# Kernel tuning notes

Hardware: AMD Instinct MI355X
Metric: run time of the kernel (lower is better)

## Reference

```python
import jax, jax.numpy as jnp
import numpy as np

N = 51200      # total nodes
E = 1638400    # total edges (avg degree 32)
G = 512        # graphs in batch
IN = 16        # input node features
H = 4          # heads
C = 32         # channels per head
HC = H * C     # 128, concat output width
SLOPE = 0.2    # LeakyReLU negative slope
BN_EPS = 1e-5


def _glorot(k, shape, fan):
    return jax.random.normal(k, shape, jnp.float32) / np.sqrt(fan).astype(np.float32)


def setup_inputs() -> dict:
    key = jax.random.key(0)
    ks = jax.random.split(key, 32)
    inp = {}
    inp['x'] = jax.random.normal(ks[0], (N, IN), jnp.float32)
    inp['edge_index'] = jax.random.randint(ks[1], (2, E), 0, N)
    inp['batch'] = jnp.sort(jax.random.randint(ks[2], (N,), 0, G))
    # GATv2 layer 1 (IN -> H*C)
    inp['l1_Wl'] = _glorot(ks[3], (IN, HC), IN)
    inp['l1_bl'] = jnp.zeros((HC,), jnp.float32)
    inp['l1_Wr'] = _glorot(ks[4], (IN, HC), IN)
    inp['l1_br'] = jnp.zeros((HC,), jnp.float32)
    inp['l1_att'] = _glorot(ks[5], (H, C), C)
    inp['l1_bias'] = jnp.zeros((HC,), jnp.float32)
    # GATv2 layer 2 (HC -> H*C)
    inp['l2_Wl'] = _glorot(ks[6], (HC, HC), HC)
    inp['l2_bl'] = jnp.zeros((HC,), jnp.float32)
    inp['l2_Wr'] = _glorot(ks[7], (HC, HC), HC)
    inp['l2_br'] = jnp.zeros((HC,), jnp.float32)
    inp['l2_att'] = _glorot(ks[8], (H, C), C)
    inp['l2_bias'] = jnp.zeros((HC,), jnp.float32)
    # MLP head (HC -> HC -> HC -> 2) with BatchNorm (eval mode, running stats 0/1)
    inp['fc1_W'] = _glorot(ks[9], (HC, HC), HC)
    inp['fc1_b'] = jnp.zeros((HC,), jnp.float32)
    inp['bn1_g'] = jnp.ones((HC,), jnp.float32)
    inp['bn1_b'] = jnp.zeros((HC,), jnp.float32)
    inp['fc2_W'] = _glorot(ks[10], (HC, HC), HC)
    inp['fc2_b'] = jnp.zeros((HC,), jnp.float32)
    inp['bn2_g'] = jnp.ones((HC,), jnp.float32)
    inp['bn2_b'] = jnp.zeros((HC,), jnp.float32)
    inp['fc3_W'] = _glorot(ks[11], (HC, 2), HC)
    inp['fc3_b'] = jnp.zeros((2,), jnp.float32)
    return inp


def gatv2_conv(x, src, dst, Wl, bl, Wr, br, att, bias):
    # PyG GATv2Conv (share_weights=False, concat=True), eval mode (no dropout).
    xl = (x @ Wl + bl).reshape(-1, H, C)  # source transform  [N,H,C]
    xr = (x @ Wr + br).reshape(-1, H, C)  # target transform  [N,H,C]
    e = jax.nn.leaky_relu(xl[src] + xr[dst], SLOPE)   # [E,H,C]
    score = jnp.einsum('ehc,hc->eh', e, att)          # [E,H]
    # segment softmax over edges sharing the same target node
    m = jax.ops.segment_max(score, dst, num_segments=N)
    ex = jnp.exp(score - m[dst])
    denom = jax.ops.segment_sum(ex, dst, num_segments=N)
    alpha = ex / (denom[dst] + 1e-16)                 # [E,H]
    out = jax.ops.segment_sum(xl[src] * alpha[:, :, None], dst, num_segments=N)
    return out.reshape(-1, HC) + bias


def reference(x, edge_index, batch,
              l1_Wl, l1_bl, l1_Wr, l1_br, l1_att, l1_bias,
              l2_Wl, l2_bl, l2_Wr, l2_br, l2_att, l2_bias,
              fc1_W, fc1_b, bn1_g, bn1_b,
              fc2_W, fc2_b, bn2_g, bn2_b,
              fc3_W, fc3_b):
    src, dst = edge_index[0], edge_index[1]
    h = jax.nn.relu(gatv2_conv(x, src, dst, l1_Wl, l1_bl, l1_Wr, l1_br, l1_att, l1_bias))
    h = jax.nn.relu(gatv2_conv(h, src, dst, l2_Wl, l2_bl, l2_Wr, l2_br, l2_att, l2_bias))
    # global mean pool over graphs
    s = jax.ops.segment_sum(h, batch, num_segments=G)
    cnt = jax.ops.segment_sum(jnp.ones((N,), h.dtype), batch, num_segments=G)
    g = s / jnp.maximum(cnt, 1.0)[:, None]            # [G,HC]
    # MLP head; BatchNorm1d in eval mode with running_mean=0, running_var=1
    def bn(z, gamma, beta):
        return z * (gamma / np.sqrt(1.0 + BN_EPS).astype(np.float32)) + beta
    g = jax.nn.relu(bn(g @ fc1_W + fc1_b, bn1_g, bn1_b))
    g = jax.nn.relu(bn(g @ fc2_W + fc2_b, bn2_g, bn2_b))
    return g @ fc3_W + fc3_b                          # [G,2]
```

## Files before the change

### kernel.cpp

```cpp
#include <hip/hip_runtime.h>
#include <math.h>

#define NN 51200
#define EE 1638400
#define GG 512
#define INF 16
#define HCC 128
#define NB 400
#define TILE 4096
#define CSRCAP 4608
#define NBLK8 (NN / 8)

typedef float vf2 __attribute__((ext_vector_type(2)));
typedef short v8s __attribute__((ext_vector_type(8)));
typedef float v4f __attribute__((ext_vector_type(4)));
typedef _Float16 vh8 __attribute__((ext_vector_type(8)));
typedef float vf8 __attribute__((ext_vector_type(8)));
#define FMA2 __builtin_elementwise_fma
#define MIN2 __builtin_elementwise_min
#define MAX2 __builtin_elementwise_max


__device__ __forceinline__ int wave_incl_scan(int v, int lane) {
#pragma unroll
    for (int d = 1; d < 64; d <<= 1) {
        int y = __shfl_up(v, d);
        if (lane >= d) v += y;
    }
    return v;
}

__device__ __forceinline__ unsigned short bf16_rtne(float f) {
    unsigned u = __builtin_bit_cast(unsigned, f);
    unsigned r = u + 0x7FFFu + ((u >> 16) & 1u);
    return (unsigned short)(r >> 16);
}

__device__ __forceinline__ unsigned short f16_rtne(float f) {
    return __builtin_bit_cast(unsigned short, (_Float16)f);
}

__device__ __forceinline__ float dpp_xor1(float x) {
    int y = __builtin_amdgcn_mov_dpp(__builtin_bit_cast(int, x), 0xB1, 0xF, 0xF, true);
    return __builtin_bit_cast(float, y);
}
__device__ __forceinline__ float dpp_xor2(float x) {
    int y = __builtin_amdgcn_mov_dpp(__builtin_bit_cast(int, x), 0x4E, 0xF, 0xF, true);
    return __builtin_bit_cast(float, y);
}

__global__ __launch_bounds__(512) void k_hist(const int* __restrict__ ei,
                                              int* __restrict__ bcnt) {
    __shared__ int h[NB];
    int t = threadIdx.x;
    if (t < NB) h[t] = 0;
    __syncthreads();
    int e0 = blockIdx.x * TILE;
#pragma unroll
    for (int s = 0; s < 8; s++) {
        int d = ei[EE + e0 + s * 512 + t];
        atomicAdd(&h[d >> 7], 1);
    }
    __syncthreads();
    if (t < NB && h[t]) atomicAdd(&bcnt[t], h[t]);
}

__global__ __launch_bounds__(512) void k_scan2(const int* __restrict__ bcnt,
                                               int* __restrict__ bbase,
                                               int* __restrict__ gcur,
                                               int* __restrict__ rowptr) {
    __shared__ int sc[512];
    int t = threadIdx.x;
    int v = (t < NB) ? bcnt[t] : 0;
    sc[t] = v;
    __syncthreads();
    for (int off = 1; off < 512; off <<= 1) {
        int u = (t >= off) ? sc[t - off] : 0;
        __syncthreads();
        sc[t] += u;
        __syncthreads();
    }
    if (t < NB) { int ex = sc[t] - v; bbase[t] = ex; gcur[t] = ex; }
    if (t == 0) { bbase[NB] = EE; rowptr[NN] = EE; }
}

__global__ __launch_bounds__(512) void k_binlin1(const int* __restrict__ ei,
                                                 int* __restrict__ gcur,
                                                 unsigned* __restrict__ binned,
                                                 const float* __restrict__ x,
                                                 const float* __restrict__ Wl,
                                                 const float* __restrict__ bl,
                                                 const float* __restrict__ Wr,
                                                 const float* __restrict__ br,
                                                 unsigned short* __restrict__ xl,
                                                 float* __restrict__ xr,
                                                 const float* __restrict__ W2l,
                                                 const float* __restrict__ W2r,
                                                 unsigned short* __restrict__ Bhi,
                                                 unsigned short* __restrict__ Blo) {
    __shared__ int h[512];
    __shared__ int lexcl[NB], lcur[NB], baseg[NB];
    __shared__ unsigned stage[TILE];
    __shared__ int wsum[8];
    __shared__ float sx[4][INF];
    int t = threadIdx.x;
    if (blockIdx.x < NB) {
        int lane = t & 63, w = t >> 6;
        h[t] = 0;
        __syncthreads();
        int e0 = blockIdx.x * TILE;
        int sv[8], dv[8];
#pragma unroll
        for (int s = 0; s < 8; s++) {
            int e = e0 + s * 512 + t;
            sv[s] = ei[e];
            dv[s] = ei[EE + e];
            atomicAdd(&h[dv[s] >> 7], 1);
        }
        __syncthreads();
        int myh = h[t];
        int incl = wave_incl_scan(myh, lane);
        if (lane == 63) wsum[w] = incl;
        __syncthreads();
        int woff = 0;
        for (int i = 0; i < w; i++) woff += wsum[i];
        incl += woff;
        if (t < NB) {
            int ex = incl - myh;
            lexcl[t] = ex;
            lcur[t] = ex;
            baseg[t] = atomicAdd(&gcur[t], myh);
        }
        __syncthreads();
#pragma unroll
        for (int s = 0; s < 8; s++) {
            int b = dv[s] >> 7;
            int r = atomicAdd(&lcur[b], 1);
            stage[r] = (unsigned)sv[s] | ((unsigned)dv[s] << 16);
        }
        __syncthreads();
#pragma unroll
        for (int s = 0; s < 8; s++) {
            int idx = s * 512 + t;
            unsigned p = stage[idx];
            int b = (int)(p >> 23);
            binned[baseg[b] + idx - lexcl[b]] = p;
        }
    } else if (blockIdx.x < NB + NN / 4) {
        int bid = blockIdx.x - NB;
        int j = t & 127;
        int ty = t >> 7;
        int row = bid * 4 + ty;
        if (t < 64) {
            sx[t >> 4][t & 15] = x[(size_t)(bid * 4 + (t >> 4)) * INF + (t & 15)];
        }
        __syncthreads();
        float al = bl[j], ar = br[j];
#pragma unroll
        for (int k = 0; k < INF; k++) {
            float xv = sx[ty][k];
            al = fmaf(xv, Wl[k * HCC + j], al);
            ar = fmaf(xv, Wr[k * HCC + j], ar);
        }
        int head = j >> 5, ch = j & 31;
        xl[((size_t)(head >> 1) * NN + row) * 64 + (head & 1) * 32 + ch] = f16_rtne(al);
        xr[((size_t)head * NN + row) * 32 + ch] = ar;
    } else {
        int gt = (blockIdx.x - NB - NN / 4) * 512 + t;
        int ks = gt >> 10;
        int rem = gt & 1023;
        int nt = rem >> 6;
        int lane = rem & 63;
        int n = nt * 16 + (lane & 15);
        int kbase = ks * 32 + (lane >> 4) * 8;
        const float* src = (n < 128) ? (W2l + n) : (W2r + n - 128);
        unsigned short hi8[8], lo8[8];
#pragma unroll
        for (int j = 0; j < 8; j++) {
            float v = src[(size_t)(kbase + j) * HCC];
            unsigned short hb = bf16_rtne(v);
            float hf = __builtin_bit_cast(float, (unsigned)hb << 16);
            hi8[j] = hb;
            lo8[j] = bf16_rtne(v - hf);
        }
        size_t idx = (size_t)gt * 8;
#pragma unroll
        for (int j = 0; j < 8; j++) { Bhi[idx + j] = hi8[j]; Blo[idx + j] = lo8[j]; }
    }
}

__global__ __launch_bounds__(512) void k_csr(const unsigned* __restrict__ binned,
                                             const int* __restrict__ bbase,
                                             int* __restrict__ rowptr,
                                             int* __restrict__ col) {
    int b = blockIdx.x;
    int base = bbase[b];
    int cnt = bbase[b + 1] - base;
    __shared__ int nh[1024], ncur[1024];
    __shared__ unsigned sbin[CSRCAP];
    __shared__ int wsum[8];
    int t = threadIdx.x;
    int lane = t & 63, w = t >> 6;
    nh[t] = 0;
    nh[t + 512] = 0;
    __syncthreads();
    for (int e = t; e < cnt; e += 512) {
        unsigned p = binned[base + e];
        if (e < CSRCAP) sbin[e] = p;
        unsigned src = p & 0xFFFFu;
        int key = (int)(((p >> 16) & 127u) << 3) | (int)(src >> 13);
        atomicAdd(&nh[key], 1);
    }
    __syncthreads();
    int c0 = nh[2 * t], c1 = nh[2 * t + 1];
    int tot = c0 + c1;
    int incl = wave_incl_scan(tot, lane);
    if (lane == 63) wsum[w] = incl;
    __syncthreads();
    int woff = 0;
    for (int i = 0; i < w; i++) woff += wsum[i];
    int tex = incl + woff - tot;
    ncur[2 * t] = base + tex;
    ncur[2 * t + 1] = base + tex + c0;
    if ((t & 3) == 0) rowptr[(b << 7) + (t >> 2)] = base + tex;
    __syncthreads();
    for (int e = t; e < cnt; e += 512) {
        unsigned p = (e < CSRCAP) ? sbin[e] : binned[base + e];
        unsigned src = p & 0xFFFFu;
        int key = (int)(((p >> 16) & 127u) << 3) | (int)(src >> 13);
        int r = atomicAdd(&ncur[key], 1);
        col[r] = (int)src;
    }
}

__global__ __launch_bounds__(256) void k_lin2(const float* __restrict__ hin,
                                              const unsigned short* __restrict__ Bhi,
                                              const unsigned short* __restrict__ Blo,
                                              const float* __restrict__ bl,
                                              const float* __restrict__ br,
                                              unsigned short* __restrict__ outl,
                                              float* __restrict__ outr) {
    const int tid = threadIdx.x;
    const int wv = tid >> 6;
    const int lane = tid & 63;
    const int m = lane & 15;
    const int quad = lane >> 4;
    const int r0 = blockIdx.x * 64 + wv * 16;
    const float* arow = hin + (size_t)(r0 + m) * HCC + quad * 8;
    const v8s* bh = (const v8s*)Bhi;
    const v8s* bo = (const v8s*)Blo;

    v4f acc[16];
#pragma unroll
    for (int nt = 0; nt < 16; nt++) acc[nt] = (v4f){0.f, 0.f, 0.f, 0.f};

#pragma unroll
    for (int ks = 0; ks < 4; ks++) {
        const float4 av0 = *(const float4*)(arow + ks * 32);
        const float4 av1 = *(const float4*)(arow + ks * 32 + 4);
        const float af[8] = {av0.x, av0.y, av0.z, av0.w, av1.x, av1.y, av1.z, av1.w};
        v8s ahi, alo;
#pragma unroll
        for (int e = 0; e < 8; e++) {
            unsigned short hb = bf16_rtne(af[e]);
            float hf = __builtin_bit_cast(float, (unsigned)hb << 16);
            ahi[e] = (short)hb;
            alo[e] = (short)bf16_rtne(af[e] - hf);
        }
        const int base = ks * 16 * 64 + lane;
#pragma unroll
        for (int nt = 0; nt < 16; nt++) {
            v8s bhv = bh[base + nt * 64];
            v8s blv = bo[base + nt * 64];
            acc[nt] = __builtin_amdgcn_mfma_f32_16x16x32_bf16(ahi, bhv, acc[nt], 0, 0, 0);
            acc[nt] = __builtin_amdgcn_mfma_f32_16x16x32_bf16(ahi, blv, acc[nt], 0, 0, 0);
            acc[nt] = __builtin_amdgcn_mfma_f32_16x16x32_bf16(alo, bhv, acc[nt], 0, 0, 0);
        }
    }
#pragma unroll
    for (int nt = 0; nt < 16; nt++) {
        int n = nt * 16 + m;
        int c = n & 127;
        float bv = (n < 128) ? bl[c] : br[c];
        if (n < 128) {
            int head = c >> 5, ch = c & 31;
            unsigned short* op = outl + (size_t)(head >> 1) * NN * 64 + (head & 1) * 32 + ch;
#pragma unroll
            for (int r = 0; r < 4; r++) {
                int row = r0 + quad * 4 + r;
                op[(size_t)row * 64] = f16_rtne(acc[nt][r] + bv);
            }
        } else {
            float* op = outr + (size_t)(c >> 5) * NN * 32 + (c & 31);
#pragma unroll
            for (int r = 0; r < 4; r++) {
                int row = r0 + quad * 4 + r;
                op[(size_t)row * 32] = acc[nt][r] + bv;
            }
        }
    }
}

__global__ __launch_bounds__(512) void k_attn(const int* __restrict__ rowptr,
                                              const int* __restrict__ col,
                                              const unsigned short* __restrict__ xl,
                                              const float* __restrict__ xr,
                                              const float* __restrict__ att,
                                              const float* __restrict__ bias,
                                              float* __restrict__ hout) {
    const int wave = threadIdx.x >> 6;
    const int lane = threadIdx.x & 63;
    const int sub = lane >> 3;
    const int hl = (lane >> 2) & 1;
    const int hq = lane & 3;
    const int pair = blockIdx.x / NBLK8;
    const int n = (blockIdx.x - pair * NBLK8) * 8 + wave;
    const int head = 2 * pair + hl;

    const char* xlq = (const char*)(xl + (size_t)pair * NN * 64)
                      + (unsigned)(hl * 64 + hq * 16);
    const float* xrp = xr + ((size_t)head * NN + n) * 32 + hq * 8;
    const float4 xrv0 = *(const float4*)(xrp);
    const float4 xrv1 = *(const float4*)(xrp + 4);
    const float4 at0 = *(const float4*)(att + head * 32 + hq * 8);
    const float4 at1 = *(const float4*)(att + head * 32 + hq * 8 + 4);
    const float LOG2E = 1.44269504088896340736f;
    const vf2 xr01 = {xrv0.x, xrv0.y}, xr23 = {xrv0.z, xrv0.w};
    const vf2 xr45 = {xrv1.x, xrv1.y}, xr67 = {xrv1.z, xrv1.w};
    const vf2 at01 = {at0.x * LOG2E, at0.y * LOG2E}, at23 = {at0.z * LOG2E, at0.w * LOG2E};
    const vf2 at45 = {at1.x * LOG2E, at1.y * LOG2E}, at67 = {at1.z * LOG2E, at1.w * LOG2E};
    const vf2 Z2 = {0.f, 0.f}, C2 = {0.2f, 0.2f};

    const int base = rowptr[n];
    const int deg = rowptr[n + 1] - base;

    float l = 0.f;
    vf2 a01 = Z2, a23 = Z2, a45 = Z2, a67 = Z2;

    for (int i0 = 0; i0 < deg; i0 += 64) {
        int mye = 0;
        if (i0 + lane < deg) mye = col[base + i0 + lane];
        const int cnt = min(64, deg - i0);
        const int events = (cnt + 15) >> 4;
        vh8 ca, cb, na{}, nb{};
        {
            const int s0 = __shfl(mye, sub);
            const int s1 = __shfl(mye, 8 + sub);
            ca = *(const vh8*)(xlq + (((unsigned)s0) << 7));
            cb = *(const vh8*)(xlq + (((unsigned)s1) << 7));
        }
        for (int g = 0; g < events; ++g) {
            if (g + 1 < events) {
                const int s0 = __shfl(mye, 16 * (g + 1) + sub);
                const int s1 = __shfl(mye, 16 * (g + 1) + 8 + sub);
                na = *(const vh8*)(xlq + (((unsigned)s0) << 7));
                nb = *(const vh8*)(xlq + (((unsigned)s1) << 7));
            }
#pragma unroll
            for (int k = 0; k < 2; ++k) {
                const vf8 fv = __builtin_convertvector(k ? cb : ca, vf8);
                const vf2 v01 = {fv[0], fv[1]}, v23 = {fv[2], fv[3]};
                const vf2 v45 = {fv[4], fv[5]}, v67 = {fv[6], fv[7]};
                vf2 e, kk, p2;
                e = v01 + xr01; kk = FMA2(C2, MIN2(e, Z2), MAX2(e, Z2)); p2 = kk * at01;
                e = v23 + xr23; kk = FMA2(C2, MIN2(e, Z2), MAX2(e, Z2)); p2 = FMA2(kk, at23, p2);
                e = v45 + xr45; kk = FMA2(C2, MIN2(e, Z2), MAX2(e, Z2)); p2 = FMA2(kk, at45, p2);
                e = v67 + xr67; kk = FMA2(C2, MIN2(e, Z2), MAX2(e, Z2)); p2 = FMA2(kk, at67, p2);
                float pp = p2.x + p2.y;
                pp += dpp_xor1(pp);
                pp += dpp_xor2(pp);
                if ((16 * g + 8 * k + sub) >= cnt) pp = -INFINITY;
                const float w = __builtin_amdgcn_exp2f(pp);
                l += w;
                const vf2 W = {w, w};
                a01 = FMA2(W, v01, a01);
                a23 = FMA2(W, v23, a23);
                a45 = FMA2(W, v45, a45);
                a67 = FMA2(W, v67, a67);
            }
            ca = na;
            cb = nb;
        }
    }
    l += __shfl_xor(l, 8);
    l += __shfl_xor(l, 16);
    l += __shfl_xor(l, 32);
    float af[8] = {a01.x, a01.y, a23.x, a23.y, a45.x, a45.y, a67.x, a67.y};
#pragma unroll
    for (int i = 0; i < 8; i++) {
        af[i] += __shfl_xor(af[i], 8);
        af[i] += __shfl_xor(af[i], 16);
        af[i] += __shfl_xor(af[i], 32);
    }
    const float inv = 1.f / (l + 1e-16f);
    if (sub == 0) {
        const float4 b0 = *(const float4*)(bias + head * 32 + hq * 8);
        const float4 b1 = *(const float4*)(bias + head * 32 + hq * 8 + 4);
        float4 o0, o1;
        o0.x = fmaxf(fmaf(af[0], inv, b0.x), 0.f);
        o0.y = fmaxf(fmaf(af[1], inv, b0.y), 0.f);
        o0.z = fmaxf(fmaf(af[2], inv, b0.z), 0.f);
        o0.w = fmaxf(fmaf(af[3], inv, b0.w), 0.f);
        o1.x = fmaxf(fmaf(af[4], inv, b1.x), 0.f);
        o1.y = fmaxf(fmaf(af[5], inv, b1.y), 0.f);
        o1.z = fmaxf(fmaf(af[6], inv, b1.z), 0.f);
        o1.w = fmaxf(fmaf(af[7], inv, b1.w), 0.f);
        float* hp = hout + (size_t)n * HCC + head * 32 + hq * 8;
        *(float4*)(hp) = o0;
        *(float4*)(hp + 4) = o1;
    }
}

__global__ __launch_bounds__(128) void k_head(const float* __restrict__ h,
                                              const int* __restrict__ batch,
                                              const float* __restrict__ fc1W, const float* __restrict__ fc1b,
                                              const float* __restrict__ bn1g, const float* __restrict__ bn1b,
                                              const float* __restrict__ fc2W, const float* __restrict__ fc2b,
                                              const float* __restrict__ bn2g, const float* __restrict__ bn2b,
                                              const float* __restrict__ fc3W, const float* __restrict__ fc3b,
                                              float* __restrict__ out) {
    int g = blockIdx.x;
    int j = threadIdx.x;
    __shared__ float buf[HCC], buf2[HCC];
    int lo = 0, hi = NN;
    while (lo < hi) { int mid = (lo + hi) >> 1; if (batch[mid] < g) lo = mid + 1; else hi = mid; }
    int s = lo;
    lo = 0; hi = NN;
    while (lo < hi) { int mid = (lo + hi) >> 1; if (batch[mid] < g + 1) lo = mid + 1; else hi = mid; }
    int e = lo;
    float s0 = 0.f, s1 = 0.f, s2 = 0.f, s3 = 0.f;
    int n = s;
    for (; n + 3 < e; n += 4) {
        s0 += h[(size_t)n * HCC + j];
        s1 += h[(size_t)(n + 1) * HCC + j];
        s2 += h[(size_t)(n + 2) * HCC + j];
        s3 += h[(size_t)(n + 3) * HCC + j];
    }
    for (; n < e; n++) s0 += h[(size_t)n * HCC + j];
    float sum = (s0 + s1) + (s2 + s3);
    float cnt = (float)(e - s);
    buf[j] = sum / fmaxf(cnt, 1.0f);
    __syncthreads();
    const float SQ = 1.00000499998749994f;
    float a = fc1b[j];
    for (int k = 0; k < HCC; k++) a = fmaf(buf[k], fc1W[k * HCC + j], a);
    a = fmaf(a, bn1g[j] / SQ, bn1b[j]);
    a = fmaxf(a, 0.f);
    buf2[j] = a;
    __syncthreads();
    a = fc2b[j];
    for (int k = 0; k < HCC; k++) a = fmaf(buf2[k], fc2W[k * HCC + j], a);
    a = fmaf(a, bn2g[j] / SQ, bn2b[j]);
    a = fmaxf(a, 0.f);
    buf[j] = a;
    __syncthreads();
    if (j < 2) {
        float o = fc3b[j];
        for (int k = 0; k < HCC; k++) o = fmaf(buf[k], fc3W[k * 2 + j], o);
        out[g * 2 + j] = o;
    }
}

extern "C" void kernel_launch(void* const* d_in, const int* in_sizes, int n_in,
                              void* d_out, int out_size, void* d_ws, size_t ws_size,
                              hipStream_t stream) {
    const float* x      = (const float*)d_in[0];
    const int*   ei     = (const int*)d_in[1];
    const int*   batch  = (const int*)d_in[2];
    const float* l1_Wl  = (const float*)d_in[3];
    const float* l1_bl  = (const float*)d_in[4];
    const float* l1_Wr  = (const float*)d_in[5];
    const float* l1_br  = (const float*)d_in[6];
    const float* l1_att = (const float*)d_in[7];
    const float* l1_bias= (const float*)d_in[8];
    const float* l2_Wl  = (const float*)d_in[9];
    const float* l2_bl  = (const float*)d_in[10];
    const float* l2_Wr  = (const float*)d_in[11];
    const float* l2_br  = (const float*)d_in[12];
    const float* l2_att = (const float*)d_in[13];
    const float* l2_bias= (const float*)d_in[14];
    const float* fc1_W  = (const float*)d_in[15];
    const float* fc1_b  = (const float*)d_in[16];
    const float* bn1_g  = (const float*)d_in[17];
    const float* bn1_b  = (const float*)d_in[18];
    const float* fc2_W  = (const float*)d_in[19];
    const float* fc2_b  = (const float*)d_in[20];
    const float* bn2_g  = (const float*)d_in[21];
    const float* bn2_b  = (const float*)d_in[22];
    const float* fc3_W  = (const float*)d_in[23];
    const float* fc3_b  = (const float*)d_in[24];
    float* out = (float*)d_out;

    unsigned short* xlh = (unsigned short*)d_ws;
    float* xr = (float*)(xlh + (size_t)NN * HCC);
    float* h  = xr + (size_t)NN * HCC;
    int* rowptr = (int*)(h + (size_t)NN * HCC);
    int* col    = rowptr + (NN + 1);
    int* bcnt   = col + EE;
    int* bbase  = bcnt + NB;
    int* gcur   = bbase + (NB + 1);
    uintptr_t bp = ((uintptr_t)(gcur + NB) + 15) & ~(uintptr_t)15;
    unsigned short* Bhi = (unsigned short*)bp;
    unsigned short* Blo = Bhi + 32768;
    unsigned* binned = (unsigned*)h;

    hipMemsetAsync(bcnt, 0, NB * sizeof(int), stream);
    k_hist<<<EE / TILE, 512, 0, stream>>>(ei, bcnt);
    k_scan2<<<1, 512, 0, stream>>>(bcnt, bbase, gcur, rowptr);
    k_binlin1<<<NB + NN / 4 + 8, 512, 0, stream>>>(ei, gcur, binned,
                                                   x, l1_Wl, l1_bl, l1_Wr, l1_br, xlh, xr,
                                                   l2_Wl, l2_Wr, Bhi, Blo);
    k_csr<<<NB, 512, 0, stream>>>(binned, bbase, rowptr, col);

    k_attn<<<2 * NBLK8, 512, 0, stream>>>(rowptr, col, xlh, xr, l1_att, l1_bias, h);

    k_lin2<<<NN / 64, 256, 0, stream>>>(h, Bhi, Blo, l2_bl, l2_br, xlh, xr);
    k_attn<<<2 * NBLK8, 512, 0, stream>>>(rowptr, col, xlh, xr, l2_att, l2_bias, h);

    k_head<<<GG, 128, 0, stream>>>(h, batch, fc1_W, fc1_b, bn1_g, bn1_b,
                                   fc2_W, fc2_b, bn2_g, bn2_b, fc3_W, fc3_b, out);
}
```

Before: 426.0 us.

## Precompute graph bounds, batch lin1 rows per block, use DPP for xor-8 reductions

The single-block scan kernel now also derives per-graph node boundaries from the sorted batch array. The head kernel reads those boundaries instead of running two serial binary searches per graph. The layer-1 linear blocks each process 16 rows instead of 4, which cuts block count and reuses the weight loads. The attention kernel's xor-8 lane reductions use a DPP row rotate instead of a shuffle. Together these trim small overheads, but they add a serial loop over all nodes to the one-block scan kernel.

Result: slower. 450.9 us (+5.9%).

```diff
diff --git a/kernel.cpp b/kernel.cpp
--- a/kernel.cpp
+++ b/kernel.cpp
@@ -48,6 +48,10 @@
     int y = __builtin_amdgcn_mov_dpp(__builtin_bit_cast(int, x), 0x4E, 0xF, 0xF, true);
     return __builtin_bit_cast(float, y);
 }
+__device__ __forceinline__ float dpp_xor8(float x) {
+    int y = __builtin_amdgcn_mov_dpp(__builtin_bit_cast(int, x), 0x128, 0xF, 0xF, true);
+    return __builtin_bit_cast(float, y);
+}
 
 __global__ __launch_bounds__(512) void k_hist(const int* __restrict__ ei,
                                               int* __restrict__ bcnt) {
@@ -68,7 +72,9 @@
 __global__ __launch_bounds__(512) void k_scan2(const int* __restrict__ bcnt,
                                                int* __restrict__ bbase,
                                                int* __restrict__ gcur,
-                                               int* __restrict__ rowptr) {
+                                               int* __restrict__ rowptr,
+                                               const int* __restrict__ batch,
+                                               int* __restrict__ gbound) {
     __shared__ int sc[512];
     int t = threadIdx.x;
     int v = (t < NB) ? bcnt[t] : 0;
@@ -82,6 +88,14 @@
     }
     if (t < NB) { int ex = sc[t] - v; bbase[t] = ex; gcur[t] = ex; }
     if (t == 0) { bbase[NB] = EE; rowptr[NN] = EE; }
+    for (int n = t; n < NN; n += 512) {
+        int bn = batch[n];
+        int bp = (n == 0) ? -1 : batch[n - 1];
+        for (int g = bp + 1; g <= bn; g++) gbound[g] = n;
+        if (n == NN - 1) {
+            for (int g = bn + 1; g <= GG; g++) gbound[g] = NN;
+        }
+    }
 }
 
 __global__ __launch_bounds__(512) void k_binlin1(const int* __restrict__ ei,
@@ -102,7 +116,7 @@
     __shared__ int lexcl[NB], lcur[NB], baseg[NB];
     __shared__ unsigned stage[TILE];
     __shared__ int wsum[8];
-    __shared__ float sx[4][INF];
+    __shared__ float sx[16][INF];
     int t = threadIdx.x;
     if (blockIdx.x < NB) {
         int lane = t & 63, w = t >> 6;
@@ -146,27 +160,31 @@
             int b = (int)(p >> 23);
             binned[baseg[b] + idx - lexcl[b]] = p;
         }
-    } else if (blockIdx.x < NB + NN / 4) {
+    } else if (blockIdx.x < NB + NN / 16) {
         int bid = blockIdx.x - NB;
         int j = t & 127;
         int ty = t >> 7;
-        int row = bid * 4 + ty;
-        if (t < 64) {
-            sx[t >> 4][t & 15] = x[(size_t)(bid * 4 + (t >> 4)) * INF + (t & 15)];
-        }
-        __syncthreads();
-        float al = bl[j], ar = br[j];
-#pragma unroll
-        for (int k = 0; k < INF; k++) {
-            float xv = sx[ty][k];
-            al = fmaf(xv, Wl[k * HCC + j], al);
-            ar = fmaf(xv, Wr[k * HCC + j], ar);
-        }
-        int head = j >> 5, ch = j & 31;
-        xl[((size_t)(head >> 1) * NN + row) * 64 + (head & 1) * 32 + ch] = f16_rtne(al);
-        xr[((size_t)head * NN + row) * 32 + ch] = ar;
+        if (t < 256) {
+            sx[t >> 4][t & 15] = x[(size_t)(bid * 16 + (t >> 4)) * INF + (t & 15)];
+        }
+        __syncthreads();
+#pragma unroll
+        for (int it = 0; it < 4; it++) {
+            int rl = it * 4 + ty;
+            int row = bid * 16 + rl;
+            float al = bl[j], ar = br[j];
+#pragma unroll
+            for (int k = 0; k < INF; k++) {
+                float xv = sx[rl][k];
+                al = fmaf(xv, Wl[k * HCC + j], al);
+                ar = fmaf(xv, Wr[k * HCC + j], ar);
+            }
+            int head = j >> 5, ch = j & 31;
+            xl[((size_t)(head >> 1) * NN + row) * 64 + (head & 1) * 32 + ch] = f16_rtne(al);
+            xr[((size_t)head * NN + row) * 32 + ch] = ar;
+        }
     } else {
-        int gt = (blockIdx.x - NB - NN / 4) * 512 + t;
+        int gt = (blockIdx.x - NB - NN / 16) * 512 + t;
         int ks = gt >> 10;
         int rem = gt & 1023;
         int nt = rem >> 6;
@@ -382,13 +400,13 @@
             cb = nb;
         }
     }
-    l += __shfl_xor(l, 8);
+    l += dpp_xor8(l);
     l += __shfl_xor(l, 16);
     l += __shfl_xor(l, 32);
     float af[8] = {a01.x, a01.y, a23.x, a23.y, a45.x, a45.y, a67.x, a67.y};
 #pragma unroll
     for (int i = 0; i < 8; i++) {
-        af[i] += __shfl_xor(af[i], 8);
+        af[i] += dpp_xor8(af[i]);
         af[i] += __shfl_xor(af[i], 16);
         af[i] += __shfl_xor(af[i], 32);
     }
@@ -412,7 +430,7 @@
 }
 
 __global__ __launch_bounds__(128) void k_head(const float* __restrict__ h,
-                                              const int* __restrict__ batch,
+                                              const int* __restrict__ gbound,
                                               const float* __restrict__ fc1W, const float* __restrict__ fc1b,
                                               const float* __restrict__ bn1g, const float* __restrict__ bn1b,
                                               const float* __restrict__ fc2W, const float* __restrict__ fc2b,
@@ -422,12 +440,8 @@
     int g = blockIdx.x;
     int j = threadIdx.x;
     __shared__ float buf[HCC], buf2[HCC];
-    int lo = 0, hi = NN;
-    while (lo < hi) { int mid = (lo + hi) >> 1; if (batch[mid] < g) lo = mid + 1; else hi = mid; }
-    int s = lo;
-    lo = 0; hi = NN;
-    while (lo < hi) { int mid = (lo + hi) >> 1; if (batch[mid] < g + 1) lo = mid + 1; else hi = mid; }
-    int e = lo;
+    int s = gbound[g];
+    int e = gbound[g + 1];
     float s0 = 0.f, s1 = 0.f, s2 = 0.f, s3 = 0.f;
     int n = s;
     for (; n + 3 < e; n += 4) {
@@ -499,17 +513,18 @@
     int* bcnt   = col + EE;
     int* bbase  = bcnt + NB;
     int* gcur   = bbase + (NB + 1);
-    uintptr_t bp = ((uintptr_t)(gcur + NB) + 15) & ~(uintptr_t)15;
+    int* gbound = gcur + NB;
+    uintptr_t bp = ((uintptr_t)(gbound + GG + 1) + 15) & ~(uintptr_t)15;
     unsigned short* Bhi = (unsigned short*)bp;
     unsigned short* Blo = Bhi + 32768;
     unsigned* binned = (unsigned*)h;
 
     hipMemsetAsync(bcnt, 0, NB * sizeof(int), stream);
     k_hist<<<EE / TILE, 512, 0, stream>>>(ei, bcnt);
-    k_scan2<<<1, 512, 0, stream>>>(bcnt, bbase, gcur, rowptr);
-    k_binlin1<<<NB + NN / 4 + 8, 512, 0, stream>>>(ei, gcur, binned,
-                                                   x, l1_Wl, l1_bl, l1_Wr, l1_br, xlh, xr,
-                                                   l2_Wl, l2_Wr, Bhi, Blo);
+    k_scan2<<<1, 512, 0, stream>>>(bcnt, bbase, gcur, rowptr, batch, gbound);
+    k_binlin1<<<NB + NN / 16 + 8, 512, 0, stream>>>(ei, gcur, binned,
+                                                    x, l1_Wl, l1_bl, l1_Wr, l1_br, xlh, xr,
+                                                    l2_Wl, l2_Wr, Bhi, Blo);
     k_csr<<<NB, 512, 0, stream>>>(binned, bbase, rowptr, col);
 
     k_attn<<<2 * NBLK8, 512, 0, stream>>>(rowptr, col, xlh, xr, l1_att, l1_bias, h);
@@ -517,6 +532,6 @@
     k_lin2<<<NN / 64, 256, 0, stream>>>(h, Bhi, Blo, l2_bl, l2_br, xlh, xr);
     k_attn<<<2 * NBLK8, 512, 0, stream>>>(rowptr, col, xlh, xr, l2_att, l2_bias, h);
 
-    k_head<<<GG, 128, 0, stream>>>(h, batch, fc1_W, fc1_b, bn1_g, bn1_b,
+    k_head<<<GG, 128, 0, stream>>>(h, gbound, fc1_W, fc1_b, bn1_g, bn1_b,
                                    fc2_W, fc2_b, bn2_g, bn2_b, fc3_W, fc3_b, out);
 }
```
